# Performance work log

Measured on AMD Instinct MI355X. Metric: run time of the kernel, lower is better.

Reference implementation:

```python
import jax, jax.numpy as jnp
import numpy as np

# Dimensions (Llama-3-8B-style GQA with paged KV cache)
B, S, HID = 1, 1024, 4096
H, HKV, D = 32, 8, 128
G = H // HKV
BLK = 16            # tokens per KV block
NB = 256            # blocks in storage
CB = 192            # context blocks attended (3072 tokens)
PAST = 2048         # tokens already cached before this step
NL = 2              # layers in kv_ptr
L = CB * BLK


def rotate_half(x):
    x1, x2 = x[..., : x.shape[-1] // 2], x[..., x.shape[-1] // 2:]
    return jnp.concatenate([-x2, x1], axis=-1)


def setup_inputs() -> dict:
    key = jax.random.key(0)
    ks = jax.random.split(key, 8)
    hidden_states = jax.random.normal(ks[0], (B, S, HID), jnp.float32)
    kv_ptr = jax.random.normal(ks[1], (NL, 2, NB, HKV, BLK, D), jnp.float32)
    Wq = 0.02 * jax.random.normal(ks[2], (H * D, HID), jnp.float32)
    Wk = 0.02 * jax.random.normal(ks[3], (HKV * D, HID), jnp.float32)
    Wv = 0.02 * jax.random.normal(ks[4], (HKV * D, HID), jnp.float32)
    Wo = 0.02 * jax.random.normal(ks[5], (HID, H * D), jnp.float32)
    # RoPE cache for the new tokens (global positions PAST..PAST+S-1), HF convention
    pos = (PAST + jnp.arange(S)).astype(jnp.float32)
    inv_freq = 1.0 / (10000.0 ** (jnp.arange(0, D, 2, dtype=jnp.float32) / D))
    freqs = pos[:, None] * inv_freq[None, :]                # [S, D/2]
    emb = jnp.concatenate([freqs, freqs], axis=-1)           # [S, D]
    cos = jnp.cos(emb)[None, None]                           # [1,1,S,D]
    sin = jnp.sin(emb)[None, None]
    new_q_lut = jnp.arange(S, dtype=jnp.int32)[None]         # identity query LUT
    new_kv_lut = (CB - S // BLK + jnp.arange(S // BLK, dtype=jnp.int32))[None]  # blocks 128..191
    all_kv_lut = jnp.arange(CB, dtype=jnp.int32)[None]       # blocks 0..191
    kv_pos = jnp.arange(L)
    q_pos = PAST + jnp.arange(S)
    mask = (kv_pos[None, None, :] <= q_pos[None, :, None])   # [1,S,L] causal over global positions
    cmd_groups = jnp.zeros((B, S), jnp.int32)                # split-K scheduling metadata (no math effect)
    return dict(hidden_states=hidden_states, kv_ptr=kv_ptr, new_q_lut=new_q_lut,
                new_kv_lut=new_kv_lut, all_kv_lut=all_kv_lut, mask=mask,
                cmd_groups=cmd_groups, cos=cos, sin=sin, Wq=Wq, Wk=Wk, Wv=Wv, Wo=Wo,
                layer_idx=0)


def reference(hidden_states, kv_ptr, new_q_lut, new_kv_lut, all_kv_lut, mask,
              cmd_groups, cos, sin, Wq, Wk, Wv, Wo, layer_idx):
    b, s, _ = hidden_states.shape
    # QKV projections (no bias)
    q = jnp.einsum('bsh,oh->bso', hidden_states, Wq).reshape(b, s, H, D).transpose(0, 2, 1, 3)
    k = jnp.einsum('bsh,oh->bso', hidden_states, Wk).reshape(b, s, HKV, D).transpose(0, 2, 1, 3)
    v = jnp.einsum('bsh,oh->bso', hidden_states, Wv).reshape(b, s, HKV, D).transpose(0, 2, 1, 3)
    # RoPE
    q = q * cos + rotate_half(q) * sin
    k = k * cos + rotate_half(k) * sin
    # fill_kv_block_storage: scatter new K/V blocks into this layer's storage (b == 1)
    kb = jnp.transpose(k[0].reshape(HKV, s // BLK, BLK, D), (1, 0, 2, 3))  # [nblk,HKV,BLK,D]
    vb = jnp.transpose(v[0].reshape(HKV, s // BLK, BLK, D), (1, 0, 2, 3))
    sk = kv_ptr[layer_idx, 0].at[new_kv_lut[0]].set(kb)
    sv = kv_ptr[layer_idx, 1].at[new_kv_lut[0]].set(vb)
    # qkv_attention: gather context blocks via LUT, masked GQA attention
    ck = jnp.transpose(sk[all_kv_lut[0]], (1, 0, 2, 3)).reshape(HKV, L, D)  # [HKV,L,D]
    cv = jnp.transpose(sv[all_kv_lut[0]], (1, 0, 2, 3)).reshape(HKV, L, D)
    qg = q[:, :, new_q_lut[0], :].reshape(b, HKV, G, s, D)
    scores = jnp.einsum('bkgsd,kld->bkgsl', qg, ck) / jnp.sqrt(jnp.float32(D))
    scores = jnp.where(mask[:, None, None], scores, jnp.finfo(scores.dtype).min)
    p = jax.nn.softmax(scores, axis=-1)
    o = jnp.einsum('bkgsl,kld->bkgsd', p, cv).reshape(b, H, s, D)
    o = o.transpose(0, 2, 1, 3).reshape(b, s, H * D)
    return jnp.einsum('bso,ho->bsh', o, Wo)
```

## Files before the change

### kernel.cpp

```cpp
#include <hip/hip_runtime.h>
#include <cstdint>
#include <cstddef>


typedef _Float16 f16;
typedef f16 f16x8 __attribute__((ext_vector_type(8)));
typedef f16 f16x4 __attribute__((ext_vector_type(4)));
typedef float f32x4 __attribute__((ext_vector_type(4)));

#define HIDN 4096
#define LCTX 3072
#define PASTN 2048
#define QK_SCALE_LOG2 0.12753102734366334f
#define RESC_THR 11.54f

__device__ __forceinline__ f32x4 mfma16(f16x8 a, f16x8 b, f32x4 c) {
    return __builtin_amdgcn_mfma_f32_16x16x32_f16(a, b, c, 0, 0, 0);
}
__device__ __forceinline__ f32x4 mfma16k16(f16x4 a, f16x4 b, f32x4 c) {
    return __builtin_amdgcn_mfma_f32_16x16x16f16(a, b, c, 0, 0, 0);
}

__device__ __forceinline__ void gl_lds16(const void* g, void* l) {
    auto gp = (const __attribute__((address_space(1))) unsigned int*)(uintptr_t)g;
    auto lp = (__attribute__((address_space(3))) unsigned int*)(uintptr_t)l;
    __builtin_amdgcn_global_load_lds(gp, lp, 16, 0, 0);
}

__device__ __forceinline__ uint32_t lds_lo(const void* p) {
    return (uint32_t)(uintptr_t)p;
}

#define TRRD(dst, va, OFF) \
    asm volatile("ds_read_b64_tr_b16 %0, %1 offset:" #OFF : "=v"(dst) : "v"(va))
#define WAITL(N) \
    asm volatile("s_waitcnt lgkmcnt(" #N ")" ::: "memory"); \
    __builtin_amdgcn_sched_barrier(0)

__global__ void cvt_h(const float* __restrict__ hidden, f16* __restrict__ h16)
{
    int i = blockIdx.x * 256 + threadIdx.x;
    f32x4 v = *(const f32x4*)(hidden + (size_t)i * 4);
    f16x4 h;
#pragma unroll
    for (int j = 0; j < 4; j++) h[j] = (f16)v[j];
    *(f16x4*)(h16 + (size_t)i * 4) = h;
}

template <int EPI, int BM>
__global__ __launch_bounds__(256, 3) void gemm_f16(
    const f16* __restrict__ A, const f16* __restrict__ Bh,
    const float* __restrict__ Bq, const float* __restrict__ Bk2,
    const float* __restrict__ Bv2,
    float* __restrict__ Cf, f16* __restrict__ Cq, f16* __restrict__ Ck,
    f16* __restrict__ Cv, int M, int N, int K,
    const float* __restrict__ kvp, const int* __restrict__ layer,
    f16* __restrict__ ckc)
{
    __shared__ f16 As[BM * 64];
    __shared__ f16 Bs[128 * 64];

    const int bx = blockIdx.x;

    if (EPI == 0 && bx >= 384) {
        const int lay = layer[0];
        int base = (bx - 384) * 256 + threadIdx.x;
#pragma unroll
        for (int pass = 0; pass < 32; ++pass) {
            int i4 = base + pass * 32768;
            int half = i4 >> 19;
            int e = (i4 & 524287) * 4;
            int hh = e >> 18, rem = e & 262143, l = rem >> 7, d = rem & 127;
            int blk = l >> 4, rr = l & 15;
            size_t src = (((size_t)(lay * 2 + half) * 256 + blk) * 8 + hh) * 2048
                       + (size_t)rr * 128 + d;
            f32x4 x = *(const f32x4*)(kvp + src);
            f16x4 h;
#pragma unroll
            for (int j = 0; j < 4; j++) h[j] = (f16)x[j];
            size_t dst = ((size_t)hh * LCTX + l) * 128 + d;
            *(f16x4*)((half ? Cv : ckc) + dst) = h;
        }
        return;
    }

    constexpr int RPW = BM / 4;
    constexpr int MI  = BM / 32;

    const int t = threadIdx.x, lane = t & 63, w = t >> 6;
    const int wm = w >> 1, wn = w & 1;
    const int l16 = lane & 15, g16 = lane >> 4;
    const int nx = (EPI == 0) ? 48 : 32;
    const int m0 = (bx / nx) * BM, n0 = (bx % nx) * 128;

    const int srow = lane >> 3;
    const int sgr  = (lane & 7) ^ srow;

    const size_t aoff = (size_t)(m0 + w * RPW + srow) * K + sgr * 8;

    const float* Bf = nullptr;
    size_t boff16 = 0;
    int nb = n0;
    if (EPI == 0) {
        if (n0 >= 5120)      { Bf = Bv2; nb = n0 - 5120; }
        else if (n0 >= 4096) { Bf = Bk2; nb = n0 - 4096; }
        else                 { Bf = Bq;  nb = n0; }
    } else {
        boff16 = (size_t)(n0 + w * 32 + srow) * K + sgr * 8;
    }
    const int brw = lane >> 4;
    const int b4  = lane & 15;
    const int bg  = b4 >> 1, bsub = (b4 & 1) << 2;

    f32x4 acc[MI][4];
#pragma unroll
    for (int i = 0; i < MI; i++)
#pragma unroll
        for (int j = 0; j < 4; j++) acc[i][j] = (f32x4){0.f, 0.f, 0.f, 0.f};

    for (int k0 = 0; k0 < K; k0 += 64) {
#pragma unroll
        for (int j = 0; j < RPW / 8; j++)
            gl_lds16(A + aoff + (size_t)j * 8 * K + k0,
                     (void*)(As + (w * RPW + j * 8) * 64));
        if (EPI == 0) {
#pragma unroll
            for (int j = 0; j < 8; j++) {
                int r = w * 32 + j * 4 + brw;
                f32x4 v = *(const f32x4*)(Bf + (size_t)(nb + r) * K + k0 + b4 * 4);
                f16x4 hv;
#pragma unroll
                for (int q = 0; q < 4; q++) hv[q] = (f16)v[q];
                *(f16x4*)&Bs[r * 64 + ((bg ^ (r & 7)) << 3) + bsub] = hv;
            }
        } else {
#pragma unroll
            for (int j = 0; j < 4; j++)
                gl_lds16(Bh + boff16 + (size_t)j * 8 * K + k0,
                         (void*)(Bs + (w * 32 + j * 8) * 64));
        }
        __syncthreads();

#pragma unroll
        for (int ks = 0; ks < 2; ks++) {
            f16x8 af[MI], bfr[4];
#pragma unroll
            for (int mi = 0; mi < MI; mi++) {
                int r = wm * (BM / 2) + mi * 16 + l16;
                int g = ks * 4 + g16;
                af[mi] = *(const f16x8*)&As[r * 64 + ((g ^ (r & 7)) << 3)];
            }
#pragma unroll
            for (int ni = 0; ni < 4; ni++) {
                int r = wn * 64 + ni * 16 + l16;
                int g = ks * 4 + g16;
                bfr[ni] = *(const f16x8*)&Bs[r * 64 + ((g ^ (r & 7)) << 3)];
            }
#pragma unroll
            for (int ni = 0; ni < 4; ni++)
#pragma unroll
                for (int mi = 0; mi < MI; mi++)
                    acc[mi][ni] = mfma16(af[mi], bfr[ni], acc[mi][ni]);
        }
        __syncthreads();
    }

#pragma unroll
    for (int mi = 0; mi < MI; mi++)
#pragma unroll
        for (int ni = 0; ni < 4; ni++)
#pragma unroll
            for (int r = 0; r < 4; r++) {
                int row = m0 + wm * (BM / 2) + mi * 16 + (g16 << 2) + r;
                int col = n0 + wn * 64 + ni * 16 + l16;
                float val = acc[mi][ni][r];
                if (EPI == 0) {
                    if (col < 4096) {
                        Cq[(size_t)row * 4096 + col] = (f16)val;
                    } else if (col < 5120) {
                        Ck[(size_t)row * 1024 + (col - 4096)] = (f16)val;
                    } else {
                        int c = col - 5120;
                        int hh = c >> 7, d = c & 127;
                        Cv[((size_t)hh * LCTX + PASTN + row) * 128 + d] = (f16)val;
                    }
                } else {
                    Cf[(size_t)row * N + col] = val;
                }
            }
}

__global__ void aux2(f16* __restrict__ q16, const f16* __restrict__ kraw,
                     const float* __restrict__ cosp, const float* __restrict__ sinp,
                     f16* __restrict__ ck)
{
    int i = blockIdx.x * 256 + threadIdx.x;
    if (i < 262144) {
        int gd = i & 7, hh = (i >> 3) & 31, s = i >> 8;
        size_t b1 = (size_t)s * 4096 + hh * 128 + gd * 8;
        f16x8 x1 = *(f16x8*)(q16 + b1);
        f16x8 x2 = *(f16x8*)(q16 + b1 + 64);
        const float* c1 = cosp + s * 128 + gd * 8;
        const float* s1 = sinp + s * 128 + gd * 8;
        f16x8 o1, o2;
#pragma unroll
        for (int j = 0; j < 8; j++) {
            float a = (float)x1[j], b = (float)x2[j];
            o1[j] = (f16)((a * c1[j] - b * s1[j]) * QK_SCALE_LOG2);
            o2[j] = (f16)((b * c1[j + 64] + a * s1[j + 64]) * QK_SCALE_LOG2);
        }
        *(f16x8*)(q16 + b1) = o1;
        *(f16x8*)(q16 + b1 + 64) = o2;
    } else {
        int ii = i - 262144;
        int gd = ii & 7, kvh = (ii >> 3) & 7, s = ii >> 6;
        size_t b1 = (size_t)s * 1024 + kvh * 128 + gd * 8;
        f16x8 x1 = *(const f16x8*)(kraw + b1);
        f16x8 x2 = *(const f16x8*)(kraw + b1 + 64);
        const float* c1 = cosp + s * 128 + gd * 8;
        const float* s1 = sinp + s * 128 + gd * 8;
        f16x8 o1, o2;
#pragma unroll
        for (int j = 0; j < 8; j++) {
            float a = (float)x1[j], b = (float)x2[j];
            o1[j] = (f16)(a * c1[j] - b * s1[j]);
            o2[j] = (f16)(b * c1[j + 64] + a * s1[j + 64]);
        }
        size_t dst = ((size_t)kvh * LCTX + PASTN + s) * 128 + gd * 8;
        *(f16x8*)(ck + dst) = o1;
        *(f16x8*)(ck + dst + 64) = o2;
    }
}

__global__ __launch_bounds__(256, 2) void attn_part(
    const f16* __restrict__ Q, const f16* __restrict__ Kc,
    const f16* __restrict__ Vc, f16* __restrict__ Op, float* __restrict__ mlb,
    const float* __restrict__ Wo, f16* __restrict__ w16)
{
    const int b = blockIdx.x;
    const int z = b >> 8;
    const int idx = b & 255;
    const int h = idx & 31;
    const int jj = idx >> 5;
    const int j = z ? (7 - jj) : jj;
    const int s0 = j * 128;
    const int kvh = h >> 2;
    const int t = threadIdx.x, lane = t & 63, w = t >> 6;
    const int l16 = lane & 15, g16 = lane >> 4;

    __shared__ f16 Ks[2][64 * 128];
    __shared__ f16 Vs[2][64 * 128];

    f16x8 qfA[4], qfB[4];
    {
        size_t baseA = (size_t)(s0 + w * 32 + l16) * 4096 + h * 128;
        size_t baseB = baseA + (size_t)16 * 4096;
#pragma unroll
        for (int kk = 0; kk < 4; kk++) {
            qfA[kk] = *(const f16x8*)(Q + baseA + kk * 32 + g16 * 8);
            qfB[kk] = *(const f16x8*)(Q + baseB + kk * 32 + g16 * 8);
        }
    }

    f32x4 ofA[8], ofB[8];
#pragma unroll
    for (int cf = 0; cf < 8; cf++) {
        ofA[cf] = (f32x4){0.f, 0.f, 0.f, 0.f};
        ofB[cf] = (f32x4){0.f, 0.f, 0.f, 0.f};
    }
    float mrA = -3.0e38f, lrA = 0.f;
    float mrB = -3.0e38f, lrB = 0.f;

    const f16* Kb = Kc + (size_t)kvh * LCTX * 128;
    const f16* Vb = Vc + (size_t)kvh * LCTX * 128;
    const int ntt = (PASTN + s0 + 128) >> 6;

    const int krow = lane >> 4;
    const int kp   = lane & 15;
    const int vrow = ((lane >> 5) << 4) + (((lane >> 3) & 3) << 2) + ((lane >> 1) & 3);
    const int vch  = (lane & 1) << 3;

    const uint32_t vs0 = lds_lo(Vs[0]) + lane * 8;
    const uint32_t vs1 = lds_lo(Vs[1]) + lane * 8;

#define STAGE_KV(l0, buf)                                                     \
    {                                                                         \
        _Pragma("unroll")                                                     \
        for (int jx = 0; jx < 4; jx++) {                                      \
            int r7 = ((jx & 1) << 2) + krow;                                  \
            int sg = kp ^ r7;                                                 \
            gl_lds16(Kb + (size_t)((l0) + w * 16 + jx * 4 + krow) * 128 + sg * 8, \
                     (void*)(Ks[buf] + (w * 16 + jx * 4) * 128));             \
        }                                                                     \
        _Pragma("unroll")                                                     \
        for (int q = 0; q < 4; q++) {                                         \
            gl_lds16(Vb + (size_t)((l0) + (q & 1) * 32 + vrow) * 128          \
                        + (w * 2 + (q >> 1)) * 16 + vch,                      \
                     (void*)(Vs[buf] + (w * 4 + q) * 512));                   \
        }                                                                     \
    }

    STAGE_KV(z * 64, 0);
    __syncthreads();

    int itp = 0;
    for (int it = z; it < ntt; it += 2, ++itp) {
        const int l0 = it << 6;
        const int cur = itp & 1;

        if (it + 2 < ntt) STAGE_KV(l0 + 128, cur ^ 1);

        f32x4 sA[4], sB[4];
#pragma unroll
        for (int ni = 0; ni < 4; ni++) {
            sA[ni] = (f32x4){0.f, 0.f, 0.f, 0.f};
            sB[ni] = (f32x4){0.f, 0.f, 0.f, 0.f};
        }
        __builtin_amdgcn_s_setprio(1);
#pragma unroll
        for (int ni = 0; ni < 4; ni++)
#pragma unroll
            for (int kk = 0; kk < 4; kk++) {
                int r = ni * 16 + l16;
                int g = kk * 4 + g16;
                f16x8 kh = *(const f16x8*)&Ks[cur][r * 128 + ((g ^ (r & 7)) << 3)];
                sA[ni] = mfma16(kh, qfA[kk], sA[ni]);
                sB[ni] = mfma16(kh, qfB[kk], sB[ni]);
            }
        __builtin_amdgcn_s_setprio(0);

#define SOFTMAX(sf, mr, lr, of, QOFF)                                          \
        {                                                                      \
            const int qrow = s0 + w * 32 + (QOFF) + l16;                       \
            if (l0 + 63 > PASTN + s0 + w * 32 + (QOFF)) {                      \
                _Pragma("unroll")                                              \
                for (int ni = 0; ni < 4; ni++)                                 \
                    _Pragma("unroll")                                          \
                    for (int r = 0; r < 4; r++) {                              \
                        int col = l0 + ni * 16 + (g16 << 2) + r;               \
                        if (col > PASTN + qrow) sf[ni][r] = -3.0e38f;          \
                    }                                                          \
            }                                                                  \
            float mx;                                                          \
            {                                                                  \
                f32x4 m4 = sf[0];                                              \
                _Pragma("unroll")                                              \
                for (int ni = 1; ni < 4; ni++) {                               \
                    m4[0] = fmaxf(m4[0], sf[ni][0]);                           \
                    m4[1] = fmaxf(m4[1], sf[ni][1]);                           \
                    m4[2] = fmaxf(m4[2], sf[ni][2]);                           \
                    m4[3] = fmaxf(m4[3], sf[ni][3]);                           \
                }                                                              \
                mx = fmaxf(fmaxf(m4[0], m4[1]), fmaxf(m4[2], m4[3]));          \
            }                                                                  \
            mx = fmaxf(mx, __shfl_xor(mx, 16));                                \
            mx = fmaxf(mx, __shfl_xor(mx, 32));                                \
            if (__any(mx > mr + RESC_THR)) {                                   \
                float mnew = fmaxf(mr, mx);                                    \
                float corr = exp2f(mr - mnew);                                 \
                mr = mnew;                                                     \
                lr *= corr;                                                    \
                float cr[4];                                                   \
                _Pragma("unroll")                                              \
                for (int r = 0; r < 4; r++) cr[r] = __shfl(corr, (g16 << 2) + r); \
                _Pragma("unroll")                                              \
                for (int cf = 0; cf < 8; cf++)                                 \
                    _Pragma("unroll")                                          \
                    for (int r = 0; r < 4; r++) of[cf][r] *= cr[r];            \
            }                                                                  \
            _Pragma("unroll")                                                  \
            for (int ni = 0; ni < 4; ni++)                                     \
                _Pragma("unroll")                                              \
                for (int r = 0; r < 4; r++) {                                  \
                    float p = exp2f(sf[ni][r] - mr);                           \
                    sf[ni][r] = p;                                             \
                    lr += p;                                                   \
                }                                                              \
        }

        SOFTMAX(sA, mrA, lrA, ofA, 0)
        SOFTMAX(sB, mrB, lrB, ofB, 16)

        f16x4 paA[4], paB[4];
#pragma unroll
        for (int ni = 0; ni < 4; ni++) {
            paA[ni][0] = (f16)sA[ni][0]; paA[ni][1] = (f16)sA[ni][1];
            paA[ni][2] = (f16)sA[ni][2]; paA[ni][3] = (f16)sA[ni][3];
            paB[ni][0] = (f16)sB[ni][0]; paB[ni][1] = (f16)sB[ni][1];
            paB[ni][2] = (f16)sB[ni][2]; paB[ni][3] = (f16)sB[ni][3];
        }

        {
            const uint32_t va = cur ? vs1 : vs0;
            f16x4 ra0, ra1, ra2, ra3, rb0, rb1, rb2, rb3;
            f16x4 rc0, rc1, rc2, rc3, rd0, rd1, rd2, rd3;
            __builtin_amdgcn_s_setprio(1);
            TRRD(ra0,va,0);     TRRD(ra1,va,512);   TRRD(ra2,va,1024);  TRRD(ra3,va,1536);
            TRRD(rb0,va,2048);  TRRD(rb1,va,2560);  TRRD(rb2,va,3072);  TRRD(rb3,va,3584);
            TRRD(rc0,va,4096);  TRRD(rc1,va,4608);  TRRD(rc2,va,5120);  TRRD(rc3,va,5632);
#define X2(cf, ni, reg) \
            ofA[cf] = mfma16k16(paA[ni], reg, ofA[cf]); \
            ofB[cf] = mfma16k16(paB[ni], reg, ofB[cf]);
            WAITL(8);
            X2(0,0,ra0) X2(0,1,ra1) X2(0,2,ra2) X2(0,3,ra3)
            TRRD(rd0,va,6144);  TRRD(rd1,va,6656);  TRRD(rd2,va,7168);  TRRD(rd3,va,7680);
            WAITL(8);
            X2(1,0,rb0) X2(1,1,rb1) X2(1,2,rb2) X2(1,3,rb3)
            TRRD(ra0,va,8192);  TRRD(ra1,va,8704);  TRRD(ra2,va,9216);  TRRD(ra3,va,9728);
            WAITL(8);
            X2(2,0,rc0) X2(2,1,rc1) X2(2,2,rc2) X2(2,3,rc3)
            TRRD(rb0,va,10240); TRRD(rb1,va,10752); TRRD(rb2,va,11264); TRRD(rb3,va,11776);
            WAITL(8);
            X2(3,0,rd0) X2(3,1,rd1) X2(3,2,rd2) X2(3,3,rd3)
            TRRD(rc0,va,12288); TRRD(rc1,va,12800); TRRD(rc2,va,13312); TRRD(rc3,va,13824);
            WAITL(8);
            X2(4,0,ra0) X2(4,1,ra1) X2(4,2,ra2) X2(4,3,ra3)
            TRRD(rd0,va,14336); TRRD(rd1,va,14848); TRRD(rd2,va,15360); TRRD(rd3,va,15872);
            WAITL(8);
            X2(5,0,rb0) X2(5,1,rb1) X2(5,2,rb2) X2(5,3,rb3)
            WAITL(4);
            X2(6,0,rc0) X2(6,1,rc1) X2(6,2,rc2) X2(6,3,rc3)
            WAITL(0);
            X2(7,0,rd0) X2(7,1,rd1) X2(7,2,rd2) X2(7,3,rd3)
#undef X2
            __builtin_amdgcn_s_setprio(0);
        }
        __syncthreads();
    }

#define WRITE_P(of, mr, lr, QOFF)                                             \
    {                                                                         \
        float l2 = lr + __shfl_xor(lr, 16);                                   \
        l2 += __shfl_xor(l2, 32);                                             \
        if (lane < 16) {                                                      \
            int srow = s0 + w * 32 + (QOFF) + lane;                           \
            *(float2*)(mlb + (((size_t)z * 1024 + srow) * 32 + h) * 2) =      \
                make_float2(mr, l2);                                          \
        }                                                                     \
        float lrr[4];                                                         \
        _Pragma("unroll")                                                     \
        for (int r = 0; r < 4; r++) lrr[r] = __shfl(l2, (g16 << 2) + r);      \
        _Pragma("unroll")                                                     \
        for (int cf = 0; cf < 8; cf++)                                        \
            _Pragma("unroll")                                                 \
            for (int r = 0; r < 4; r++) {                                     \
                int srow = s0 + w * 32 + (QOFF) + (g16 << 2) + r;             \
                int d = cf * 16 + l16;                                        \
                Op[(size_t)z * 4194304 + (size_t)srow * 4096                  \
                   + (size_t)h * 128 + d] = (f16)(of[cf][r] / lrr[r]);        \
            }                                                                 \
    }
    WRITE_P(ofA, mrA, lrA, 0)
    WRITE_P(ofB, mrB, lrB, 16)
#undef WRITE_P
#undef SOFTMAX
#undef STAGE_KV

    if (j < 4) {
        int js  = z ? (jj - 4) : jj;
        int cid = h * 8 + js * 2 + z;
        const float* src = Wo + (size_t)cid * 65536;
        f16* dst = w16 + (size_t)cid * 65536;
#pragma unroll 4
        for (int p = 0; p < 64; ++p) {
            int e = (p * 256 + t) * 4;
            f32x4 v = *(const f32x4*)(src + e);
            f16x4 hv;
#pragma unroll
            for (int jx = 0; jx < 4; jx++) hv[jx] = (f16)v[jx];
            *(f16x4*)(dst + e) = hv;
        }
    }
}

__global__ void attn_combine(const f16* __restrict__ Op, const float* __restrict__ mlb,
                             f16* __restrict__ obuf)
{
    int i = blockIdx.x * 256 + threadIdx.x;
    int d8 = i & 15, hh = (i >> 4) & 31, s = i >> 9;
    float2 ml0 = *(const float2*)(mlb + (((size_t)0 * 1024 + s) * 32 + hh) * 2);
    float2 ml1 = *(const float2*)(mlb + (((size_t)1 * 1024 + s) * 32 + hh) * 2);
    float mstar = fmaxf(ml0.x, ml1.x);
    float w0 = exp2f(ml0.x - mstar) * ml0.y;
    float w1 = exp2f(ml1.x - mstar) * ml1.y;
    float inv = 1.0f / (w0 + w1);
    size_t off = (size_t)s * 4096 + (size_t)hh * 128 + d8 * 8;
    f16x8 a = *(const f16x8*)(Op + off);
    f16x8 b = *(const f16x8*)(Op + 4194304 + off);
    f16x8 o;
#pragma unroll
    for (int jx = 0; jx < 8; jx++)
        o[jx] = (f16)(((float)a[jx] * w0 + (float)b[jx] * w1) * inv);
    *(f16x8*)(obuf + off) = o;
}

extern "C" void kernel_launch(void* const* d_in, const int* in_sizes, int n_in,
                              void* d_out, int out_size, void* d_ws, size_t ws_size,
                              hipStream_t stream)
{
    const float* hidden = (const float*)d_in[0];
    const float* kvp    = (const float*)d_in[1];
    const float* cosp   = (const float*)d_in[7];
    const float* sinp   = (const float*)d_in[8];
    const float* Wq     = (const float*)d_in[9];
    const float* Wk     = (const float*)d_in[10];
    const float* Wv     = (const float*)d_in[11];
    const float* Wo     = (const float*)d_in[12];
    const int*   layer  = (const int*)d_in[13];

    char* ws = (char*)d_ws;
    f16* w16  = (f16*)ws;
    f16* opart= (f16*)(ws + 33554432);
    f16* h16  = (f16*)(ws + 50331648);
    f16* ck   = (f16*)(ws + 58720256);
    f16* cv   = (f16*)(ws + 65011712);
    f16* obuf = (f16*)(ws + 71303168);

    f16*   q16  = (f16*)d_out;
    f16*   kraw = (f16*)((char*)d_out + 8388608);
    float* mlb  = (float*)((char*)d_out + 8388608);

    cvt_h<<<4096, 256, 0, stream>>>(hidden, h16);

    gemm_f16<0, 128><<<dim3(512), 256, 0, stream>>>(
        h16, nullptr, Wq, Wk, Wv, nullptr, q16, kraw, cv, 1024, 6144, 4096,
        kvp, layer, ck);

    aux2<<<1280, 256, 0, stream>>>(q16, kraw, cosp, sinp, ck);

    attn_part<<<dim3(512), 256, 0, stream>>>(q16, ck, cv, opart, mlb, Wo, w16);

    attn_combine<<<2048, 256, 0, stream>>>(opart, mlb, obuf);

    gemm_f16<1, 64><<<dim3(512), 256, 0, stream>>>(
        obuf, w16, nullptr, nullptr, nullptr, (float*)d_out, nullptr, nullptr,
        nullptr, 1024, 4096, 4096, nullptr, nullptr, nullptr);
}
```

Before: 262.0 us.

## Double-buffer LDS and prefetch fp32 weights in QKV GEMM main loop

Adds double-buffered LDS tiles to the fused QKV projection GEMM (EPI==0). While the current tile is consumed, it prefetches the next A tile via direct global-to-LDS loads and the next fp32 weight tile into registers, then converts and stores the weights after the MFMA work. One of the two barriers per iteration goes away, and global load latency is meant to overlap with compute. In exchange LDS use doubles and register pressure rises, so launch bounds for this variant drop to 2 blocks per CU, lowering occupancy.

```diff
diff --git a/kernel.cpp b/kernel.cpp
--- a/kernel.cpp
+++ b/kernel.cpp
@@ -48,7 +48,7 @@
 }
 
 template <int EPI, int BM>
-__global__ __launch_bounds__(256, 3) void gemm_f16(
+__global__ __launch_bounds__(256, EPI == 0 ? 2 : 3) void gemm_f16(
     const f16* __restrict__ A, const f16* __restrict__ Bh,
     const float* __restrict__ Bq, const float* __restrict__ Bk2,
     const float* __restrict__ Bv2,
@@ -57,8 +57,8 @@
     const float* __restrict__ kvp, const int* __restrict__ layer,
     f16* __restrict__ ckc)
 {
-    __shared__ f16 As[BM * 64];
-    __shared__ f16 Bs[128 * 64];
+    __shared__ f16 As[(EPI == 0 ? 2 : 1) * BM * 64];
+    __shared__ f16 Bs[(EPI == 0 ? 2 : 1) * 128 * 64];
 
     const int bx = blockIdx.x;
 
@@ -98,71 +98,128 @@
 
     const size_t aoff = (size_t)(m0 + w * RPW + srow) * K + sgr * 8;
 
-    const float* Bf = nullptr;
-    size_t boff16 = 0;
-    int nb = n0;
+    f32x4 acc[MI][4];
+#pragma unroll
+    for (int i = 0; i < MI; i++)
+#pragma unroll
+        for (int j = 0; j < 4; j++) acc[i][j] = (f32x4){0.f, 0.f, 0.f, 0.f};
+
     if (EPI == 0) {
+        const float* Bf;
+        int nb = n0;
         if (n0 >= 5120)      { Bf = Bv2; nb = n0 - 5120; }
         else if (n0 >= 4096) { Bf = Bk2; nb = n0 - 4096; }
-        else                 { Bf = Bq;  nb = n0; }
+        else                 { Bf = Bq; }
+        const int brw = lane >> 4;
+        const int b4  = lane & 15;
+        const int bg  = b4 >> 1, bsub = (b4 & 1) << 2;
+        const float* bbase = Bf + (size_t)(nb + w * 32 + brw) * K + b4 * 4;
+
+        int bwr[8];
+#pragma unroll
+        for (int j = 0; j < 8; j++) {
+            int r = w * 32 + j * 4 + brw;
+            bwr[j] = r * 64 + ((bg ^ (r & 7)) << 3) + bsub;
+        }
+
+        f32x4 bv[8];
+#pragma unroll
+        for (int j = 0; j < 8; j++)
+            bv[j] = *(const f32x4*)(bbase + (size_t)(j * 4) * K);
+#pragma unroll
+        for (int j = 0; j < 4; j++)
+            gl_lds16(A + aoff + (size_t)j * 8 * K,
+                     (void*)(As + (w * 32 + j * 8) * 64));
+#pragma unroll
+        for (int j = 0; j < 8; j++) {
+            f16x4 hv;
+#pragma unroll
+            for (int q = 0; q < 4; q++) hv[q] = (f16)bv[j][q];
+            *(f16x4*)&Bs[bwr[j]] = hv;
+        }
+        __syncthreads();
+
+        for (int k0 = 0; k0 < K; k0 += 64) {
+            const int cur = (k0 >> 6) & 1;
+            const int nxt = cur ^ 1;
+            const bool more = (k0 + 64 < K);
+            if (more) {
+#pragma unroll
+                for (int j = 0; j < 4; j++)
+                    gl_lds16(A + aoff + (size_t)j * 8 * K + k0 + 64,
+                             (void*)(As + nxt * (BM * 64) + (w * 32 + j * 8) * 64));
+#pragma unroll
+                for (int j = 0; j < 8; j++)
+                    bv[j] = *(const f32x4*)(bbase + (size_t)(j * 4) * K + k0 + 64);
+            }
+#pragma unroll
+            for (int ks = 0; ks < 2; ks++) {
+                f16x8 af[MI], bfr[4];
+#pragma unroll
+                for (int mi = 0; mi < MI; mi++) {
+                    int r = wm * (BM / 2) + mi * 16 + l16;
+                    int g = ks * 4 + g16;
+                    af[mi] = *(const f16x8*)&As[cur * (BM * 64) + r * 64 + ((g ^ (r & 7)) << 3)];
+                }
+#pragma unroll
+                for (int ni = 0; ni < 4; ni++) {
+                    int r = wn * 64 + ni * 16 + l16;
+                    int g = ks * 4 + g16;
+                    bfr[ni] = *(const f16x8*)&Bs[cur * 8192 + r * 64 + ((g ^ (r & 7)) << 3)];
+                }
+#pragma unroll
+                for (int ni = 0; ni < 4; ni++)
+#pragma unroll
+                    for (int mi = 0; mi < MI; mi++)
+                        acc[mi][ni] = mfma16(af[mi], bfr[ni], acc[mi][ni]);
+            }
+            if (more) {
+#pragma unroll
+                for (int j = 0; j < 8; j++) {
+                    f16x4 hv;
+#pragma unroll
+                    for (int q = 0; q < 4; q++) hv[q] = (f16)bv[j][q];
+                    *(f16x4*)&Bs[nxt * 8192 + bwr[j]] = hv;
+                }
+            }
+            __syncthreads();
+        }
     } else {
-        boff16 = (size_t)(n0 + w * 32 + srow) * K + sgr * 8;
-    }
-    const int brw = lane >> 4;
-    const int b4  = lane & 15;
-    const int bg  = b4 >> 1, bsub = (b4 & 1) << 2;
-
-    f32x4 acc[MI][4];
-#pragma unroll
-    for (int i = 0; i < MI; i++)
-#pragma unroll
-        for (int j = 0; j < 4; j++) acc[i][j] = (f32x4){0.f, 0.f, 0.f, 0.f};
-
-    for (int k0 = 0; k0 < K; k0 += 64) {
-#pragma unroll
-        for (int j = 0; j < RPW / 8; j++)
-            gl_lds16(A + aoff + (size_t)j * 8 * K + k0,
-                     (void*)(As + (w * RPW + j * 8) * 64));
-        if (EPI == 0) {
-#pragma unroll
-            for (int j = 0; j < 8; j++) {
-                int r = w * 32 + j * 4 + brw;
-                f32x4 v = *(const f32x4*)(Bf + (size_t)(nb + r) * K + k0 + b4 * 4);
-                f16x4 hv;
-#pragma unroll
-                for (int q = 0; q < 4; q++) hv[q] = (f16)v[q];
-                *(f16x4*)&Bs[r * 64 + ((bg ^ (r & 7)) << 3) + bsub] = hv;
-            }
-        } else {
+        const size_t boff16 = (size_t)(n0 + w * 32 + srow) * K + sgr * 8;
+        for (int k0 = 0; k0 < K; k0 += 64) {
+#pragma unroll
+            for (int j = 0; j < RPW / 8; j++)
+                gl_lds16(A + aoff + (size_t)j * 8 * K + k0,
+                         (void*)(As + (w * RPW + j * 8) * 64));
 #pragma unroll
             for (int j = 0; j < 4; j++)
                 gl_lds16(Bh + boff16 + (size_t)j * 8 * K + k0,
                          (void*)(Bs + (w * 32 + j * 8) * 64));
-        }
-        __syncthreads();
-
-#pragma unroll
-        for (int ks = 0; ks < 2; ks++) {
-            f16x8 af[MI], bfr[4];
-#pragma unroll
-            for (int mi = 0; mi < MI; mi++) {
-                int r = wm * (BM / 2) + mi * 16 + l16;
-                int g = ks * 4 + g16;
-                af[mi] = *(const f16x8*)&As[r * 64 + ((g ^ (r & 7)) << 3)];
+            __syncthreads();
+
+#pragma unroll
+            for (int ks = 0; ks < 2; ks++) {
+                f16x8 af[MI], bfr[4];
+#pragma unroll
+                for (int mi = 0; mi < MI; mi++) {
+                    int r = wm * (BM / 2) + mi * 16 + l16;
+                    int g = ks * 4 + g16;
+                    af[mi] = *(const f16x8*)&As[r * 64 + ((g ^ (r & 7)) << 3)];
+                }
+#pragma unroll
+                for (int ni = 0; ni < 4; ni++) {
+                    int r = wn * 64 + ni * 16 + l16;
+                    int g = ks * 4 + g16;
+                    bfr[ni] = *(const f16x8*)&Bs[r * 64 + ((g ^ (r & 7)) << 3)];
+                }
+#pragma unroll
+                for (int ni = 0; ni < 4; ni++)
+#pragma unroll
+                    for (int mi = 0; mi < MI; mi++)
+                        acc[mi][ni] = mfma16(af[mi], bfr[ni], acc[mi][ni]);
             }
-#pragma unroll
-            for (int ni = 0; ni < 4; ni++) {
-                int r = wn * 64 + ni * 16 + l16;
-                int g = ks * 4 + g16;
-                bfr[ni] = *(const f16x8*)&Bs[r * 64 + ((g ^ (r & 7)) << 3)];
-            }
-#pragma unroll
-            for (int ni = 0; ni < 4; ni++)
-#pragma unroll
-                for (int mi = 0; mi < MI; mi++)
-                    acc[mi][ni] = mfma16(af[mi], bfr[ni], acc[mi][ni]);
-        }
-        __syncthreads();
+            __syncthreads();
+        }
     }
 
 #pragma unroll
```

Result: faster. 246.5 us (-5.9%).

## Double-buffer LDS and register-prefetch fp32 weights in QKV projection GEMM

Applied to the files above, without the earlier changes.

The QKV GEMM path (EPI==0) now uses two LDS buffers for A and B plus two register sets of prefetched fp32 weight tiles. Each iteration issues global loads for the next tiles while running MFMAs on the current buffer, with a single barrier per half-step. The goal is to hide global-memory latency from the fp32 weight reads and their conversion. In exchange it doubles LDS use and raises register pressure, which is why launch bounds drop to 2 waves per SIMD and occupancy falls.

```diff
diff --git a/kernel.cpp b/kernel.cpp
--- a/kernel.cpp
+++ b/kernel.cpp
@@ -48,7 +48,7 @@
 }
 
 template <int EPI, int BM>
-__global__ __launch_bounds__(256, 3) void gemm_f16(
+__global__ __launch_bounds__(256, EPI == 0 ? 2 : 3) void gemm_f16(
     const f16* __restrict__ A, const f16* __restrict__ Bh,
     const float* __restrict__ Bq, const float* __restrict__ Bk2,
     const float* __restrict__ Bv2,
@@ -57,8 +57,8 @@
     const float* __restrict__ kvp, const int* __restrict__ layer,
     f16* __restrict__ ckc)
 {
-    __shared__ f16 As[BM * 64];
-    __shared__ f16 Bs[128 * 64];
+    __shared__ f16 As[(EPI == 0 ? 2 : 1) * BM * 64];
+    __shared__ f16 Bs[(EPI == 0 ? 2 : 1) * 128 * 64];
 
     const int bx = blockIdx.x;
 
@@ -98,71 +98,118 @@
 
     const size_t aoff = (size_t)(m0 + w * RPW + srow) * K + sgr * 8;
 
-    const float* Bf = nullptr;
-    size_t boff16 = 0;
-    int nb = n0;
+    f32x4 acc[MI][4];
+#pragma unroll
+    for (int i = 0; i < MI; i++)
+#pragma unroll
+        for (int j = 0; j < 4; j++) acc[i][j] = (f32x4){0.f, 0.f, 0.f, 0.f};
+
     if (EPI == 0) {
+        const float* Bf;
+        int nb = n0;
         if (n0 >= 5120)      { Bf = Bv2; nb = n0 - 5120; }
         else if (n0 >= 4096) { Bf = Bk2; nb = n0 - 4096; }
-        else                 { Bf = Bq;  nb = n0; }
+        else                 { Bf = Bq; }
+        const int brw = lane >> 4;
+        const int b4  = lane & 15;
+        const int bg  = b4 >> 1, bsub = (b4 & 1) << 2;
+        const float* bbase = Bf + (size_t)(nb + w * 32 + brw) * K + b4 * 4;
+
+        int bwr[8];
+#pragma unroll
+        for (int j = 0; j < 8; j++) {
+            int r = w * 32 + j * 4 + brw;
+            bwr[j] = r * 64 + ((bg ^ (r & 7)) << 3) + bsub;
+        }
+
+        f32x4 bvA[8], bvB[8];
+
+#define LOADB(dst, kk) { _Pragma("unroll") for (int j = 0; j < 8; j++) \
+        dst[j] = *(const f32x4*)(bbase + (size_t)(j * 4) * K + (kk)); }
+#define LOADA(kk, buf) { _Pragma("unroll") for (int j = 0; j < 4; j++) \
+        gl_lds16(A + aoff + (size_t)j * 8 * K + (kk), \
+                 (void*)(As + (buf) * (BM * 64) + (w * 32 + j * 8) * 64)); }
+#define WRITEB(src, buf) { _Pragma("unroll") for (int j = 0; j < 8; j++) { \
+        f16x4 hv; _Pragma("unroll") for (int q = 0; q < 4; q++) hv[q] = (f16)src[j][q]; \
+        *(f16x4*)&Bs[(buf) * 8192 + bwr[j]] = hv; } }
+#define MFMAT(buf) { _Pragma("unroll") for (int ks = 0; ks < 2; ks++) { \
+        f16x8 af[MI], bfr[4]; \
+        _Pragma("unroll") for (int mi = 0; mi < MI; mi++) { \
+            int r = wm * (BM / 2) + mi * 16 + l16; int g = ks * 4 + g16; \
+            af[mi] = *(const f16x8*)&As[(buf) * (BM * 64) + r * 64 + ((g ^ (r & 7)) << 3)]; } \
+        _Pragma("unroll") for (int ni = 0; ni < 4; ni++) { \
+            int r = wn * 64 + ni * 16 + l16; int g = ks * 4 + g16; \
+            bfr[ni] = *(const f16x8*)&Bs[(buf) * 8192 + r * 64 + ((g ^ (r & 7)) << 3)]; } \
+        _Pragma("unroll") for (int ni = 0; ni < 4; ni++) \
+            _Pragma("unroll") for (int mi = 0; mi < MI; mi++) \
+                acc[mi][ni] = mfma16(af[mi], bfr[ni], acc[mi][ni]); } }
+#define GBAR(VM) \
+        asm volatile("s_waitcnt lgkmcnt(0)" ::: "memory"); \
+        asm volatile("s_waitcnt vmcnt(" #VM ")" ::: "memory"); \
+        __builtin_amdgcn_s_barrier(); \
+        __builtin_amdgcn_sched_barrier(0);
+
+        LOADA(0, 0);
+        LOADB(bvA, 0);
+        WRITEB(bvA, 0);
+        LOADB(bvB, 64);
+        GBAR(8)
+
+        for (int k0 = 0; k0 < K; k0 += 128) {
+            const int kb2 = (k0 + 128 < K) ? k0 + 128 : K - 64;
+            const int kb3 = (k0 + 192 < K) ? k0 + 192 : K - 64;
+            LOADA(k0 + 64, 1);
+            LOADB(bvA, kb2);
+            MFMAT(0);
+            WRITEB(bvB, 1);
+            GBAR(8)
+            LOADA(kb2, 0);
+            LOADB(bvB, kb3);
+            MFMAT(1);
+            WRITEB(bvA, 0);
+            GBAR(8)
+        }
+#undef LOADB
+#undef LOADA
+#undef WRITEB
+#undef MFMAT
+#undef GBAR
     } else {
-        boff16 = (size_t)(n0 + w * 32 + srow) * K + sgr * 8;
-    }
-    const int brw = lane >> 4;
-    const int b4  = lane & 15;
-    const int bg  = b4 >> 1, bsub = (b4 & 1) << 2;
-
-    f32x4 acc[MI][4];
-#pragma unroll
-    for (int i = 0; i < MI; i++)
-#pragma unroll
-        for (int j = 0; j < 4; j++) acc[i][j] = (f32x4){0.f, 0.f, 0.f, 0.f};
-
-    for (int k0 = 0; k0 < K; k0 += 64) {
-#pragma unroll
-        for (int j = 0; j < RPW / 8; j++)
-            gl_lds16(A + aoff + (size_t)j * 8 * K + k0,
-                     (void*)(As + (w * RPW + j * 8) * 64));
-        if (EPI == 0) {
-#pragma unroll
-            for (int j = 0; j < 8; j++) {
-                int r = w * 32 + j * 4 + brw;
-                f32x4 v = *(const f32x4*)(Bf + (size_t)(nb + r) * K + k0 + b4 * 4);
-                f16x4 hv;
-#pragma unroll
-                for (int q = 0; q < 4; q++) hv[q] = (f16)v[q];
-                *(f16x4*)&Bs[r * 64 + ((bg ^ (r & 7)) << 3) + bsub] = hv;
-            }
-        } else {
+        const size_t boff16 = (size_t)(n0 + w * 32 + srow) * K + sgr * 8;
+        for (int k0 = 0; k0 < K; k0 += 64) {
+#pragma unroll
+            for (int j = 0; j < RPW / 8; j++)
+                gl_lds16(A + aoff + (size_t)j * 8 * K + k0,
+                         (void*)(As + (w * RPW + j * 8) * 64));
 #pragma unroll
             for (int j = 0; j < 4; j++)
                 gl_lds16(Bh + boff16 + (size_t)j * 8 * K + k0,
                          (void*)(Bs + (w * 32 + j * 8) * 64));
-        }
-        __syncthreads();
-
-#pragma unroll
-        for (int ks = 0; ks < 2; ks++) {
-            f16x8 af[MI], bfr[4];
-#pragma unroll
-            for (int mi = 0; mi < MI; mi++) {
-                int r = wm * (BM / 2) + mi * 16 + l16;
-                int g = ks * 4 + g16;
-                af[mi] = *(const f16x8*)&As[r * 64 + ((g ^ (r & 7)) << 3)];
+            __syncthreads();
+
+#pragma unroll
+            for (int ks = 0; ks < 2; ks++) {
+                f16x8 af[MI], bfr[4];
+#pragma unroll
+                for (int mi = 0; mi < MI; mi++) {
+                    int r = wm * (BM / 2) + mi * 16 + l16;
+                    int g = ks * 4 + g16;
+                    af[mi] = *(const f16x8*)&As[r * 64 + ((g ^ (r & 7)) << 3)];
+                }
+#pragma unroll
+                for (int ni = 0; ni < 4; ni++) {
+                    int r = wn * 64 + ni * 16 + l16;
+                    int g = ks * 4 + g16;
+                    bfr[ni] = *(const f16x8*)&Bs[r * 64 + ((g ^ (r & 7)) << 3)];
+                }
+#pragma unroll
+                for (int ni = 0; ni < 4; ni++)
+#pragma unroll
+                    for (int mi = 0; mi < MI; mi++)
+                        acc[mi][ni] = mfma16(af[mi], bfr[ni], acc[mi][ni]);
             }
-#pragma unroll
-            for (int ni = 0; ni < 4; ni++) {
-                int r = wn * 64 + ni * 16 + l16;
-                int g = ks * 4 + g16;
-                bfr[ni] = *(const f16x8*)&Bs[r * 64 + ((g ^ (r & 7)) << 3)];
-            }
-#pragma unroll
-            for (int ni = 0; ni < 4; ni++)
-#pragma unroll
-                for (int mi = 0; mi < MI; mi++)
-                    acc[mi][ni] = mfma16(af[mi], bfr[ni], acc[mi][ni]);
-        }
-        __syncthreads();
+            __syncthreads();
+        }
     }
 
 #pragma unroll
```

After: 251.2 us. 1.04x faster.
